# Performance work log

Measured on AMD Instinct MI355X. Metric: run time of the kernel, lower is better.

## Reference

```python
import jax, jax.numpy as jnp
import numpy as np

N = 100000   # nodes
E = 1600000  # edges
D = 128      # input feature dim
H = 128      # hidden dim
C = 40       # output classes


def _gcn_conv(x, W, b, src, dst, norm):
    # PyG GCNConv: h = x @ W; out_i = sum_j (d_i^-1/2 d_j^-1/2) h_j over in-edges,
    # including self-loops, then + bias. norm = deg^-1/2 with self-loop-augmented degree.
    h = x @ W                                    # [N, H]
    coef = norm[src] * norm[dst]                 # [E]
    agg = jax.ops.segment_sum(h[src] * coef[:, None], dst, num_segments=N)
    agg = agg + h * (norm * norm)[:, None]       # self-loop term
    return agg + b


def setup_inputs() -> dict:
    key = jax.random.key(0)
    ks = jax.random.split(key, 12)
    x = jax.random.normal(ks[0], (N, D), dtype=jnp.float32)
    edge_index = jax.random.randint(ks[1], (2, E), 0, N, dtype=jnp.int64)

    def lin(k, fan_in, fan_out):
        s = 1.0 / np.sqrt(fan_in)
        return jax.random.uniform(k, (fan_in, fan_out), jnp.float32, -s, s)

    return {
        "x": x,
        "edge_index": edge_index,
        "W1": lin(ks[2], D, H), "b1": jnp.zeros((H,), jnp.float32),
        "W2": lin(ks[3], H, H), "b2": jnp.zeros((H,), jnp.float32),
        "W3": lin(ks[4], H, H), "b3": jnp.zeros((H,), jnp.float32),
        "Wp1": lin(ks[5], H, H), "bp1": jnp.zeros((H,), jnp.float32),
        "Wp2": lin(ks[6], H, C), "bp2": jnp.zeros((C,), jnp.float32),
    }


def reference(x, edge_index, W1, b1, W2, b2, W3, b3, Wp1, bp1, Wp2, bp2):
    src, dst = edge_index[0], edge_index[1]
    # degree with self-loops (GCNConv adds self-loops by default)
    deg = jax.ops.segment_sum(jnp.ones((E,), jnp.float32), dst, num_segments=N) + 1.0
    norm = jax.lax.rsqrt(deg)                    # deg^-1/2

    h = x
    for W, b in ((W1, b1), (W2, b2), (W3, b3)):
        h = _gcn_conv(h, W, b, src, dst, norm)
        h = jax.nn.relu(h)
        # dropout is a no-op at inference / rate 0

    h = h @ Wp1 + bp1
    h = h @ Wp2 + bp2
    return jax.nn.log_softmax(h, axis=1)
```

## Files before the change

### kernel.cpp

```cpp
#include <hip/hip_runtime.h>
#include <hip/hip_bf16.h>
#include <math.h>


#define DH 128
#define NC 40
#define BN 256
#define MAXNB 512
#define CH 8192
#define ECAP 6144
#define SP 136

typedef __attribute__((ext_vector_type(8))) short bf16x8;
typedef __attribute__((ext_vector_type(4))) float f32x4;

__device__ __forceinline__ unsigned short f2bf(float f) {
    unsigned u = __float_as_uint(f);
    unsigned r = (u + 0x7fffu + ((u >> 16) & 1u)) >> 16;
    return (unsigned short)r;
}
__device__ __forceinline__ unsigned pack2(float lo, float hi) {
    return (unsigned)f2bf(lo) | ((unsigned)f2bf(hi) << 16);
}


__global__ __launch_bounds__(256) void bucket_hist(const int* __restrict__ dst, int E,
                                                   unsigned* __restrict__ bcnt) {
    __shared__ unsigned h[MAXNB];
    int tid = threadIdx.x;
    for (int i = tid; i < MAXNB; i += 256) h[i] = 0;
    __syncthreads();
    int e0 = blockIdx.x * CH;
    int e1 = min(e0 + CH, E);
    for (int i = e0 + tid; i < e1; i += 256)
        atomicAdd(&h[dst[i] >> 8], 1u);
    __syncthreads();
    for (int i = tid; i < MAXNB; i += 256)
        if (h[i]) atomicAdd(&bcnt[i], h[i]);
}

__global__ __launch_bounds__(256) void bucket_alloc(const unsigned* __restrict__ bcnt,
                                                    unsigned* __restrict__ bbase,
                                                    unsigned* __restrict__ bpos,
                                                    unsigned* __restrict__ cursor, int NB) {
    int i = blockIdx.x * 256 + threadIdx.x;
    if (i < NB) {
        unsigned c = bcnt[i];
        unsigned o = atomicAdd(cursor, c);
        bbase[i] = o;
        bpos[i] = o;
    }
}

__global__ __launch_bounds__(256) void bucket_scatter(const int* __restrict__ src,
                                                      const int* __restrict__ dst, int E,
                                                      unsigned* __restrict__ bpos,
                                                      unsigned* __restrict__ ebuf) {
    __shared__ unsigned hist[MAXNB];
    __shared__ unsigned lbase[MAXNB];
    __shared__ unsigned gbase[MAXNB];
    __shared__ unsigned cur[MAXNB];
    __shared__ unsigned sorted[CH];
    __shared__ unsigned short sbkt[CH];
    __shared__ unsigned total;

    int tid = threadIdx.x;
    int e0 = blockIdx.x * CH;
    int nE = min(CH, E - e0);

    for (int i = tid; i < MAXNB; i += 256) { hist[i] = 0; cur[i] = 0; }
    if (tid == 0) total = 0;
    __syncthreads();

    for (int i = tid; i < nE; i += 256)
        atomicAdd(&hist[dst[e0 + i] >> 8], 1u);
    __syncthreads();

    for (int i = tid; i < MAXNB; i += 256) {
        unsigned h = hist[i];
        lbase[i] = h ? atomicAdd(&total, h) : 0u;
        gbase[i] = h ? atomicAdd(&bpos[i], h) : 0u;
    }
    __syncthreads();

    for (int i = tid; i < nE; i += 256) {
        int s = src[e0 + i];
        int d = dst[e0 + i];
        unsigned b = (unsigned)d >> 8;
        unsigned r = atomicAdd(&cur[b], 1u);
        unsigned p = lbase[b] + r;
        sorted[p] = ((unsigned)s << 8) | ((unsigned)d & 255u);
        sbkt[p] = (unsigned short)b;
    }
    __syncthreads();

    for (int p = tid; p < nE; p += 256) {
        unsigned b = sbkt[p];
        ebuf[gbase[b] + (p - lbase[b])] = sorted[p];
    }
}


__global__ __launch_bounds__(256) void bucket_deg(const unsigned* __restrict__ ebuf,
                                                  const unsigned* __restrict__ bbase,
                                                  const unsigned* __restrict__ bcnt,
                                                  unsigned* __restrict__ cnt,
                                                  float* __restrict__ nrm,
                                                  unsigned* __restrict__ dh, int N) {
    __shared__ unsigned h[BN];
    __shared__ unsigned dhh[256];
    int b = blockIdx.x, tid = threadIdx.x;
    unsigned ebase = bbase[b], ecnt = bcnt[b];
    h[tid] = 0; dhh[tid] = 0;
    __syncthreads();
    for (unsigned i = tid; i < ecnt; i += 256)
        atomicAdd(&h[ebuf[ebase + i] & 255u], 1u);
    __syncthreads();
    int node = b * BN + tid;
    unsigned myh = h[tid];
    if (node < N) {
        cnt[node] = myh;
        nrm[node] = rsqrtf((float)myh + 1.0f);
        atomicAdd(&dhh[min(myh, 255u)], 1u);
    }
    __syncthreads();
    if (dhh[tid]) atomicAdd(&dh[tid], dhh[tid]);
}

__global__ __launch_bounds__(256) void deg_scan(const unsigned* __restrict__ dh,
                                                unsigned* __restrict__ binpos,
                                                unsigned* __restrict__ nstart0,
                                                unsigned* __restrict__ estart) {
    __shared__ unsigned s[256];
    int t = threadIdx.x;
    s[t] = dh[t];
    __syncthreads();
    unsigned ns = 0, es = 0;
    for (int d = t + 1; d < 256; ++d) { ns += s[d]; es += s[d] * (unsigned)d; }
    binpos[t] = ns;
    nstart0[t] = ns;
    estart[t] = es;
}

__global__ __launch_bounds__(256) void deg_scatter(const unsigned* __restrict__ cnt, int N,
                                                   unsigned* __restrict__ binpos,
                                                   const unsigned* __restrict__ nstart0,
                                                   const unsigned* __restrict__ estart,
                                                   int* __restrict__ perm,
                                                   unsigned* __restrict__ pd2,
                                                   unsigned* __restrict__ offN) {
    __shared__ unsigned h[256], base[256], cur[256], sns[256], ses[256];
    int t = threadIdx.x;
    h[t] = 0; cur[t] = 0; sns[t] = nstart0[t]; ses[t] = estart[t];
    __syncthreads();
    int i = blockIdx.x * 256 + t;
    unsigned d = 0;
    if (i < N) { d = min(cnt[i], 255u); atomicAdd(&h[d], 1u); }
    __syncthreads();
    if (h[t]) base[t] = atomicAdd(&binpos[t], h[t]);
    __syncthreads();
    if (i < N) {
        unsigned r = atomicAdd(&cur[d], 1u);
        unsigned idx = base[d] + r;
        unsigned off2 = ses[d] + (idx - sns[d]) * d;
        perm[idx] = i;
        pd2[idx] = (off2 << 9) | d;
        offN[i] = off2;
    }
}


__global__ __launch_bounds__(256) void bucket_fill(const unsigned* __restrict__ ebuf,
                                                   const unsigned* __restrict__ bbase,
                                                   const unsigned* __restrict__ bcnt,
                                                   const unsigned* __restrict__ offN,
                                                   int* __restrict__ csr, int N) {
    __shared__ unsigned h[BN], lb[BN], cur[BN], ofs[BN];
    __shared__ int lcsr[ECAP];
    __shared__ unsigned char snl[ECAP];
    __shared__ unsigned tot;

    int b = blockIdx.x, tid = threadIdx.x;
    unsigned ebase = bbase[b], ecnt = bcnt[b];
    int node = b * BN + tid;
    h[tid] = 0; cur[tid] = 0;
    ofs[tid] = (node < N) ? offN[node] : 0u;
    if (tid == 0) tot = 0;
    __syncthreads();

    for (unsigned i = tid; i < ecnt; i += 256)
        atomicAdd(&h[ebuf[ebase + i] & 255u], 1u);
    __syncthreads();

    unsigned myh = h[tid];
    lb[tid] = myh ? atomicAdd(&tot, myh) : 0u;
    __syncthreads();

    if (ecnt <= ECAP) {
        for (unsigned i = tid; i < ecnt; i += 256) {
            unsigned v = ebuf[ebase + i];
            unsigned nl = v & 255u;
            unsigned r = atomicAdd(&cur[nl], 1u);
            unsigned p = lb[nl] + r;
            lcsr[p] = (int)(v >> 8);
            snl[p] = (unsigned char)nl;
        }
        __syncthreads();
        for (unsigned i = tid; i < ecnt; i += 256) {
            unsigned nl = snl[i];
            csr[ofs[nl] + (i - lb[nl])] = lcsr[i];
        }
    } else {
        for (unsigned i = tid; i < ecnt; i += 256) {
            unsigned v = ebuf[ebase + i];
            unsigned nl = v & 255u;
            unsigned r = atomicAdd(&cur[nl], 1u);
            csr[ofs[nl] + r] = (int)(v >> 8);
        }
    }
}


__global__ __launch_bounds__(256) void prep_w(const float* __restrict__ W1,
                                              const float* __restrict__ W2,
                                              const float* __restrict__ W3,
                                              const float* __restrict__ Wp1,
                                              const float* __restrict__ bp1,
                                              const float* __restrict__ Wp2,
                                              const float* __restrict__ bp2,
                                              unsigned short* __restrict__ Wt,
                                              unsigned short* __restrict__ Wft,
                                              float* __restrict__ bfh) {
    int id = blockIdx.x * 256 + threadIdx.x;
    if (id < 3 * DH * DH) {
        int l = id >> 14, r = id & (DH * DH - 1);
        int k = r >> 7, n = r & 127;
        const float* W = (l == 0) ? W1 : (l == 1) ? W2 : W3;
        Wt[l * DH * DH + n * DH + k] = f2bf(W[k * DH + n]);
    } else if (id < 3 * DH * DH + 48 * DH) {
        int o = id - 3 * DH * DH;
        int c = o >> 7, k = o & 127;
        float acc = 0.f;
        if (c < NC)
            for (int j = 0; j < DH; ++j) acc += Wp1[k * DH + j] * Wp2[j * NC + c];
        Wft[c * DH + k] = f2bf(acc);
    } else if (id < 3 * DH * DH + 48 * DH + 48) {
        int c = id - 3 * DH * DH - 48 * DH;
        float acc = 0.f;
        if (c < NC) {
            acc = bp2[c];
            for (int j = 0; j < DH; ++j) acc += bp1[j] * Wp2[j * NC + c];
        }
        bfh[c] = acc;
    }
}


__global__ __launch_bounds__(256) void gemm_mfma_f32(const float* __restrict__ X,
                                                     const unsigned short* __restrict__ Wt,
                                                     const float* __restrict__ nrm,
                                                     unsigned short* __restrict__ outb,
                                                     int nrows) {
    const int tid = threadIdx.x;
    const int wave = tid >> 6;
    const int lane = tid & 63;
    const int m = lane & 15;
    const int quad = lane >> 4;
    const int rbase = blockIdx.x * 128 + wave * 32;

    union U8 { bf16x8 v; unsigned u[4]; };

    f32x4 acc[2][8];
#pragma unroll
    for (int rt = 0; rt < 2; ++rt)
#pragma unroll
        for (int ct = 0; ct < 8; ++ct) acc[rt][ct] = (f32x4){0.f, 0.f, 0.f, 0.f};

#pragma unroll
    for (int kt = 0; kt < 4; ++kt) {
        const int kof = kt * 32 + quad * 8;
        bf16x8 a[2], b[8];
#pragma unroll
        for (int rt = 0; rt < 2; ++rt) {
            int r = rbase + rt * 16 + m;
            r = (r < nrows) ? r : (nrows - 1);
            const float* p = X + (size_t)r * DH + kof;
            float4 u0 = *(const float4*)p;
            float4 u1 = *(const float4*)(p + 4);
            U8 t;
            t.u[0] = pack2(u0.x, u0.y);
            t.u[1] = pack2(u0.z, u0.w);
            t.u[2] = pack2(u1.x, u1.y);
            t.u[3] = pack2(u1.z, u1.w);
            a[rt] = t.v;
        }
#pragma unroll
        for (int ct = 0; ct < 8; ++ct)
            b[ct] = *(const bf16x8*)(Wt + (ct * 16 + m) * DH + kof);
#pragma unroll
        for (int rt = 0; rt < 2; ++rt)
#pragma unroll
            for (int ct = 0; ct < 8; ++ct)
                acc[rt][ct] = __builtin_amdgcn_mfma_f32_16x16x32_bf16(a[rt], b[ct], acc[rt][ct], 0, 0, 0);
    }

#pragma unroll
    for (int rt = 0; rt < 2; ++rt)
#pragma unroll
        for (int reg = 0; reg < 4; ++reg) {
            int r = rbase + rt * 16 + quad * 4 + reg;
            if (r < nrows) {
                float s = nrm[r];
#pragma unroll
                for (int ct = 0; ct < 8; ++ct)
                    outb[(size_t)r * DH + ct * 16 + m] = f2bf(acc[rt][ct][reg] * s);
            }
        }
}


__device__ __forceinline__ void bf8_add(float* acc, uint4 v) {
    acc[0] += __uint_as_float(v.x << 16);
    acc[1] += __uint_as_float(v.x & 0xffff0000u);
    acc[2] += __uint_as_float(v.y << 16);
    acc[3] += __uint_as_float(v.y & 0xffff0000u);
    acc[4] += __uint_as_float(v.z << 16);
    acc[5] += __uint_as_float(v.z & 0xffff0000u);
    acc[6] += __uint_as_float(v.w << 16);
    acc[7] += __uint_as_float(v.w & 0xffff0000u);
}

__device__ __forceinline__ void gather_phase(const uint4* __restrict__ Abf,
                                             const int* __restrict__ csr,
                                             const unsigned* __restrict__ pd2,
                                             const int* __restrict__ perm,
                                             const float* __restrict__ bias,
                                             unsigned short (*sA)[SP],
                                             int* snode, float* snrm, int N) {
    const int tid = threadIdx.x;
    const int g = tid >> 4;
    const int lane = tid & 15;
    const int idx = blockIdx.x * 16 + g;
    if (idx < N) {
        const unsigned pd = pd2[idx];
        const unsigned o = pd >> 9;
        const unsigned d = pd & 511u;
        const int node = perm[idx];

        float acc[8];
        {
            uint4 v = Abf[(size_t)node * 16 + lane];
            acc[0] = __uint_as_float(v.x << 16);
            acc[1] = __uint_as_float(v.x & 0xffff0000u);
            acc[2] = __uint_as_float(v.y << 16);
            acc[3] = __uint_as_float(v.y & 0xffff0000u);
            acc[4] = __uint_as_float(v.z << 16);
            acc[5] = __uint_as_float(v.z & 0xffff0000u);
            acc[6] = __uint_as_float(v.w << 16);
            acc[7] = __uint_as_float(v.w & 0xffff0000u);
        }

        unsigned e = 0;
        for (; e + 4 <= d; e += 4) {
            int s0 = csr[o + e + 0];
            int s1 = csr[o + e + 1];
            int s2 = csr[o + e + 2];
            int s3 = csr[o + e + 3];
            uint4 v0 = Abf[(size_t)s0 * 16 + lane];
            uint4 v1 = Abf[(size_t)s1 * 16 + lane];
            uint4 v2 = Abf[(size_t)s2 * 16 + lane];
            uint4 v3 = Abf[(size_t)s3 * 16 + lane];
            bf8_add(acc, v0);
            bf8_add(acc, v1);
            bf8_add(acc, v2);
            bf8_add(acc, v3);
        }
        for (; e < d; ++e) {
            int s = csr[o + e];
            uint4 v = Abf[(size_t)s * 16 + lane];
            bf8_add(acc, v);
        }

        float nm = rsqrtf((float)d + 1.0f);
        if (lane == 0) { snode[g] = node; snrm[g] = nm; }
        float4 b0 = *(const float4*)(bias + lane * 8);
        float4 b1 = *(const float4*)(bias + lane * 8 + 4);
        uint4 ov;
        ov.x = pack2(fmaxf(acc[0] * nm + b0.x, 0.f), fmaxf(acc[1] * nm + b0.y, 0.f));
        ov.y = pack2(fmaxf(acc[2] * nm + b0.z, 0.f), fmaxf(acc[3] * nm + b0.w, 0.f));
        ov.z = pack2(fmaxf(acc[4] * nm + b1.x, 0.f), fmaxf(acc[5] * nm + b1.y, 0.f));
        ov.w = pack2(fmaxf(acc[6] * nm + b1.z, 0.f), fmaxf(acc[7] * nm + b1.w, 0.f));
        *(uint4*)&sA[g][lane * 8] = ov;
    }
    __syncthreads();
}


__global__ __launch_bounds__(256) void agg_gemm(const uint4* __restrict__ Abf,
                                                const int* __restrict__ csr,
                                                const unsigned* __restrict__ pd2,
                                                const int* __restrict__ perm,
                                                const float* __restrict__ bias,
                                                const unsigned short* __restrict__ Wt,
                                                unsigned short* __restrict__ outb, int N) {
    __shared__ unsigned short sA[16][SP];
    __shared__ int snode[16];
    __shared__ float snrm[16];
    gather_phase(Abf, csr, pd2, perm, bias, sA, snode, snrm, N);

    const int tid = threadIdx.x;
    const int wave = tid >> 6;
    const int l64 = tid & 63;
    const int m = l64 & 15;
    const int quad = l64 >> 4;

    f32x4 acc[2];
    acc[0] = (f32x4){0.f, 0.f, 0.f, 0.f};
    acc[1] = (f32x4){0.f, 0.f, 0.f, 0.f};

#pragma unroll
    for (int kt = 0; kt < 4; ++kt) {
        const int kof = kt * 32 + quad * 8;
        bf16x8 a = *(const bf16x8*)&sA[m][kof];
#pragma unroll
        for (int c2 = 0; c2 < 2; ++c2) {
            const int ct = wave * 2 + c2;
            bf16x8 b = *(const bf16x8*)(Wt + (ct * 16 + m) * DH + kof);
            acc[c2] = __builtin_amdgcn_mfma_f32_16x16x32_bf16(a, b, acc[c2], 0, 0, 0);
        }
    }

#pragma unroll
    for (int reg = 0; reg < 4; ++reg) {
        int idx = blockIdx.x * 16 + quad * 4 + reg;
        if (idx < N) {
            int r = snode[quad * 4 + reg];
            float s = snrm[quad * 4 + reg];
#pragma unroll
            for (int c2 = 0; c2 < 2; ++c2)
                outb[(size_t)r * DH + (wave * 2 + c2) * 16 + m] = f2bf(acc[c2][reg] * s);
        }
    }
}


__global__ __launch_bounds__(256) void agg_head(const uint4* __restrict__ Abf,
                                                const int* __restrict__ csr,
                                                const unsigned* __restrict__ pd2,
                                                const int* __restrict__ perm,
                                                const float* __restrict__ bias,
                                                const unsigned short* __restrict__ Wft,
                                                const float* __restrict__ bfh,
                                                float* __restrict__ out, int N) {
    __shared__ unsigned short sA[16][SP];
    __shared__ int snode[16];
    __shared__ float snrm[16];
    gather_phase(Abf, csr, pd2, perm, bias, sA, snode, snrm, N);

    const int tid = threadIdx.x;
    if (tid >= 64) return;
    const int m = tid & 15;
    const int quad = tid >> 4;

    f32x4 acc[3];
#pragma unroll
    for (int ct = 0; ct < 3; ++ct) acc[ct] = (f32x4){0.f, 0.f, 0.f, 0.f};

#pragma unroll
    for (int kt = 0; kt < 4; ++kt) {
        const int kof = kt * 32 + quad * 8;
        bf16x8 a = *(const bf16x8*)&sA[m][kof];
#pragma unroll
        for (int ct = 0; ct < 3; ++ct) {
            bf16x8 b = *(const bf16x8*)(Wft + (ct * 16 + m) * DH + kof);
            acc[ct] = __builtin_amdgcn_mfma_f32_16x16x32_bf16(a, b, acc[ct], 0, 0, 0);
        }
    }

    float bias0 = bfh[m];
    float bias1 = bfh[16 + m];
    float bias2 = bfh[32 + m];

#pragma unroll
    for (int reg = 0; reg < 4; ++reg) {
        float v0 = acc[0][reg] + bias0;
        float v1 = acc[1][reg] + bias1;
        float v2 = (m < 8) ? (acc[2][reg] + bias2) : -1e30f;
        float mx = fmaxf(fmaxf(v0, v1), v2);
#pragma unroll
        for (int dlt = 1; dlt < 16; dlt <<= 1) mx = fmaxf(mx, __shfl_xor(mx, dlt));
        float s = __expf(v0 - mx) + __expf(v1 - mx) + ((m < 8) ? __expf(v2 - mx) : 0.f);
#pragma unroll
        for (int dlt = 1; dlt < 16; dlt <<= 1) s += __shfl_xor(s, dlt);
        float ls = mx + __logf(s);
        int idx = blockIdx.x * 16 + quad * 4 + reg;
        if (idx < N) {
            int r = snode[quad * 4 + reg];
            out[(size_t)r * NC + m] = v0 - ls;
            out[(size_t)r * NC + 16 + m] = v1 - ls;
            if (m < 8) out[(size_t)r * NC + 32 + m] = v2 - ls;
        }
    }
}


extern "C" void kernel_launch(void* const* d_in, const int* in_sizes, int n_in,
                              void* d_out, int out_size, void* d_ws, size_t ws_size,
                              hipStream_t stream) {
    const float* x   = (const float*)d_in[0];
    const int*   ei  = (const int*)d_in[1];
    const float* W1  = (const float*)d_in[2];
    const float* b1  = (const float*)d_in[3];
    const float* W2  = (const float*)d_in[4];
    const float* b2  = (const float*)d_in[5];
    const float* W3  = (const float*)d_in[6];
    const float* b3  = (const float*)d_in[7];
    const float* Wp1 = (const float*)d_in[8];
    const float* bp1 = (const float*)d_in[9];
    const float* Wp2 = (const float*)d_in[10];
    const float* bp2 = (const float*)d_in[11];
    float* out = (float*)d_out;

    const int N = in_sizes[0] / DH;
    const int E = in_sizes[1] / 2;
    const int* src = ei;
    const int* dst = ei + E;
    const int NB = (N + BN - 1) / BN;

    char* w = (char*)d_ws;
    unsigned short* Ab  = (unsigned short*)w; w += (size_t)N * DH * 2;
    unsigned short* Bb  = (unsigned short*)w; w += (size_t)N * DH * 2;
    int*      csr    = (int*)w;      w += (size_t)E * 4;
    unsigned* ebuf   = (unsigned*)w; w += (size_t)E * 4;
    unsigned* bcnt   = (unsigned*)w; w += MAXNB * 4;
    unsigned* cursor = (unsigned*)w; w += 16;
    unsigned* dh     = (unsigned*)w; w += 256 * 4;
    unsigned* bbase  = (unsigned*)w; w += MAXNB * 4;
    unsigned* bpos   = (unsigned*)w; w += MAXNB * 4;
    unsigned* binpos = (unsigned*)w; w += 256 * 4;
    unsigned* nstart0= (unsigned*)w; w += 256 * 4;
    unsigned* estart = (unsigned*)w; w += 256 * 4;
    unsigned* cnt    = (unsigned*)w; w += (size_t)N * 4;
    float*    nrm    = (float*)w;    w += (size_t)N * 4;
    unsigned* offN   = (unsigned*)w; w += (size_t)N * 4;
    unsigned* pd2    = (unsigned*)w; w += (size_t)((N + 31) & ~31) * 4;
    int*      perm   = (int*)w;      w += (size_t)((N + 31) & ~31) * 4;
    unsigned short* Wt  = (unsigned short*)w; w += 3 * DH * DH * 2;
    unsigned short* Wft = (unsigned short*)w; w += 48 * DH * 2;
    float*    bfh    = (float*)w;    w += 64 * 4;

    const int gC = (E + CH - 1) / CH;
    const int gN = (N + 255) / 256;

    hipMemsetAsync(bcnt, 0, MAXNB * 4 + 16 + 256 * 4, stream);
    bucket_hist   <<<gC, 256, 0, stream>>>(dst, E, bcnt);
    bucket_alloc  <<<(NB + 255) / 256, 256, 0, stream>>>(bcnt, bbase, bpos, cursor, NB);
    bucket_scatter<<<gC, 256, 0, stream>>>(src, dst, E, bpos, ebuf);
    bucket_deg    <<<NB, 256, 0, stream>>>(ebuf, bbase, bcnt, cnt, nrm, dh, N);
    deg_scan      <<<1, 256, 0, stream>>>(dh, binpos, nstart0, estart);
    deg_scatter   <<<gN, 256, 0, stream>>>(cnt, N, binpos, nstart0, estart, perm, pd2, offN);
    bucket_fill   <<<NB, 256, 0, stream>>>(ebuf, bbase, bcnt, offN, csr, N);
    prep_w<<<(3 * DH * DH + 48 * DH + 48 + 255) / 256, 256, 0, stream>>>(
        W1, W2, W3, Wp1, bp1, Wp2, bp2, Wt, Wft, bfh);

    const int gG = (N + 127) / 128;
    const int gF = (N + 15) / 16;

    gemm_mfma_f32<<<gG, 256, 0, stream>>>(x, Wt, nrm, Ab, N);
    agg_gemm<<<gF, 256, 0, stream>>>((const uint4*)Ab, csr, pd2, perm, b1,
                                     Wt + DH * DH, Bb, N);
    agg_gemm<<<gF, 256, 0, stream>>>((const uint4*)Bb, csr, pd2, perm, b2,
                                     Wt + 2 * DH * DH, Ab, N);
    agg_head<<<gF, 256, 0, stream>>>((const uint4*)Ab, csr, pd2, perm, b3,
                                     Wft, bfh, out, N);
}
```

Measured before the change: 418.0 us.

## Replace bucketed two-pass CSR build with direct global-atomic degree count and scatter

The old CSR build bucketed edges by destination block in shared memory, wrote an intermediate edge buffer, and then did per-bucket degree and fill passes. The new build counts degrees with global atomics per edge and scatters source indices into the CSR using an atomic cursor per node. This drops the ebuf round trip and several kernel launches. In exchange it relies on contended global atomics with random access, and neighbour order inside each row becomes nondeterministic, which can change float summation order. offN is now consumed as a cursor, so it ends pointing at row ends, while pd2 still holds the row starts.

```diff
diff --git a/kernel.cpp b/kernel.cpp
--- a/kernel.cpp
+++ b/kernel.cpp
@@ -5,10 +5,6 @@
 
 #define DH 128
 #define NC 40
-#define BN 256
-#define MAXNB 512
-#define CH 8192
-#define ECAP 6144
 #define SP 136
 
 typedef __attribute__((ext_vector_type(8))) short bf16x8;
@@ -24,107 +20,30 @@
 }
 
 
-__global__ __launch_bounds__(256) void bucket_hist(const int* __restrict__ dst, int E,
-                                                   unsigned* __restrict__ bcnt) {
-    __shared__ unsigned h[MAXNB];
-    int tid = threadIdx.x;
-    for (int i = tid; i < MAXNB; i += 256) h[i] = 0;
-    __syncthreads();
-    int e0 = blockIdx.x * CH;
-    int e1 = min(e0 + CH, E);
-    for (int i = e0 + tid; i < e1; i += 256)
-        atomicAdd(&h[dst[i] >> 8], 1u);
-    __syncthreads();
-    for (int i = tid; i < MAXNB; i += 256)
-        if (h[i]) atomicAdd(&bcnt[i], h[i]);
-}
-
-__global__ __launch_bounds__(256) void bucket_alloc(const unsigned* __restrict__ bcnt,
-                                                    unsigned* __restrict__ bbase,
-                                                    unsigned* __restrict__ bpos,
-                                                    unsigned* __restrict__ cursor, int NB) {
+__global__ __launch_bounds__(256) void edge_deg(const int* __restrict__ dst, int E,
+                                                unsigned* __restrict__ cnt) {
     int i = blockIdx.x * 256 + threadIdx.x;
-    if (i < NB) {
-        unsigned c = bcnt[i];
-        unsigned o = atomicAdd(cursor, c);
-        bbase[i] = o;
-        bpos[i] = o;
-    }
-}
-
-__global__ __launch_bounds__(256) void bucket_scatter(const int* __restrict__ src,
-                                                      const int* __restrict__ dst, int E,
-                                                      unsigned* __restrict__ bpos,
-                                                      unsigned* __restrict__ ebuf) {
-    __shared__ unsigned hist[MAXNB];
-    __shared__ unsigned lbase[MAXNB];
-    __shared__ unsigned gbase[MAXNB];
-    __shared__ unsigned cur[MAXNB];
-    __shared__ unsigned sorted[CH];
-    __shared__ unsigned short sbkt[CH];
-    __shared__ unsigned total;
-
-    int tid = threadIdx.x;
-    int e0 = blockIdx.x * CH;
-    int nE = min(CH, E - e0);
-
-    for (int i = tid; i < MAXNB; i += 256) { hist[i] = 0; cur[i] = 0; }
-    if (tid == 0) total = 0;
-    __syncthreads();
-
-    for (int i = tid; i < nE; i += 256)
-        atomicAdd(&hist[dst[e0 + i] >> 8], 1u);
-    __syncthreads();
-
-    for (int i = tid; i < MAXNB; i += 256) {
-        unsigned h = hist[i];
-        lbase[i] = h ? atomicAdd(&total, h) : 0u;
-        gbase[i] = h ? atomicAdd(&bpos[i], h) : 0u;
-    }
-    __syncthreads();
-
-    for (int i = tid; i < nE; i += 256) {
-        int s = src[e0 + i];
-        int d = dst[e0 + i];
-        unsigned b = (unsigned)d >> 8;
-        unsigned r = atomicAdd(&cur[b], 1u);
-        unsigned p = lbase[b] + r;
-        sorted[p] = ((unsigned)s << 8) | ((unsigned)d & 255u);
-        sbkt[p] = (unsigned short)b;
-    }
-    __syncthreads();
-
-    for (int p = tid; p < nE; p += 256) {
-        unsigned b = sbkt[p];
-        ebuf[gbase[b] + (p - lbase[b])] = sorted[p];
-    }
-}
-
-
-__global__ __launch_bounds__(256) void bucket_deg(const unsigned* __restrict__ ebuf,
-                                                  const unsigned* __restrict__ bbase,
-                                                  const unsigned* __restrict__ bcnt,
-                                                  unsigned* __restrict__ cnt,
+    int stride = gridDim.x * 256;
+    for (; i < E; i += stride)
+        atomicAdd(&cnt[dst[i]], 1u);
+}
+
+
+__global__ __launch_bounds__(256) void node_stats(const unsigned* __restrict__ cnt,
                                                   float* __restrict__ nrm,
                                                   unsigned* __restrict__ dh, int N) {
-    __shared__ unsigned h[BN];
     __shared__ unsigned dhh[256];
-    int b = blockIdx.x, tid = threadIdx.x;
-    unsigned ebase = bbase[b], ecnt = bcnt[b];
-    h[tid] = 0; dhh[tid] = 0;
-    __syncthreads();
-    for (unsigned i = tid; i < ecnt; i += 256)
-        atomicAdd(&h[ebuf[ebase + i] & 255u], 1u);
-    __syncthreads();
-    int node = b * BN + tid;
-    unsigned myh = h[tid];
-    if (node < N) {
-        cnt[node] = myh;
-        nrm[node] = rsqrtf((float)myh + 1.0f);
-        atomicAdd(&dhh[min(myh, 255u)], 1u);
-    }
-    __syncthreads();
-    if (dhh[tid]) atomicAdd(&dh[tid], dhh[tid]);
+    int t = threadIdx.x;
+    dhh[t] = 0;
+    __syncthreads();
+    int i = blockIdx.x * 256 + t;
+    if (i < N) {
+        unsigned c = cnt[i];
+        nrm[i] = rsqrtf((float)c + 1.0f);
+        atomicAdd(&dhh[min(c, 255u)], 1u);
+    }
+    __syncthreads();
+    if (dhh[t]) atomicAdd(&dh[t], dhh[t]);
 }
 
 __global__ __launch_bounds__(256) void deg_scan(const unsigned* __restrict__ dh,
@@ -170,53 +89,15 @@
 }
 
 
-__global__ __launch_bounds__(256) void bucket_fill(const unsigned* __restrict__ ebuf,
-                                                   const unsigned* __restrict__ bbase,
-                                                   const unsigned* __restrict__ bcnt,
-                                                   const unsigned* __restrict__ offN,
-                                                   int* __restrict__ csr, int N) {
-    __shared__ unsigned h[BN], lb[BN], cur[BN], ofs[BN];
-    __shared__ int lcsr[ECAP];
-    __shared__ unsigned char snl[ECAP];
-    __shared__ unsigned tot;
-
-    int b = blockIdx.x, tid = threadIdx.x;
-    unsigned ebase = bbase[b], ecnt = bcnt[b];
-    int node = b * BN + tid;
-    h[tid] = 0; cur[tid] = 0;
-    ofs[tid] = (node < N) ? offN[node] : 0u;
-    if (tid == 0) tot = 0;
-    __syncthreads();
-
-    for (unsigned i = tid; i < ecnt; i += 256)
-        atomicAdd(&h[ebuf[ebase + i] & 255u], 1u);
-    __syncthreads();
-
-    unsigned myh = h[tid];
-    lb[tid] = myh ? atomicAdd(&tot, myh) : 0u;
-    __syncthreads();
-
-    if (ecnt <= ECAP) {
-        for (unsigned i = tid; i < ecnt; i += 256) {
-            unsigned v = ebuf[ebase + i];
-            unsigned nl = v & 255u;
-            unsigned r = atomicAdd(&cur[nl], 1u);
-            unsigned p = lb[nl] + r;
-            lcsr[p] = (int)(v >> 8);
-            snl[p] = (unsigned char)nl;
-        }
-        __syncthreads();
-        for (unsigned i = tid; i < ecnt; i += 256) {
-            unsigned nl = snl[i];
-            csr[ofs[nl] + (i - lb[nl])] = lcsr[i];
-        }
-    } else {
-        for (unsigned i = tid; i < ecnt; i += 256) {
-            unsigned v = ebuf[ebase + i];
-            unsigned nl = v & 255u;
-            unsigned r = atomicAdd(&cur[nl], 1u);
-            csr[ofs[nl] + r] = (int)(v >> 8);
-        }
+__global__ __launch_bounds__(256) void csr_scatter(const int* __restrict__ src,
+                                                   const int* __restrict__ dst, int E,
+                                                   unsigned* __restrict__ offN,
+                                                   int* __restrict__ csr) {
+    int i = blockIdx.x * 256 + threadIdx.x;
+    int stride = gridDim.x * 256;
+    for (; i < E; i += stride) {
+        unsigned p = atomicAdd(&offN[dst[i]], 1u);
+        csr[p] = src[i];
     }
 }
 
@@ -525,23 +406,17 @@
     const int E = in_sizes[1] / 2;
     const int* src = ei;
     const int* dst = ei + E;
-    const int NB = (N + BN - 1) / BN;
 
     char* w = (char*)d_ws;
     unsigned short* Ab  = (unsigned short*)w; w += (size_t)N * DH * 2;
     unsigned short* Bb  = (unsigned short*)w; w += (size_t)N * DH * 2;
     int*      csr    = (int*)w;      w += (size_t)E * 4;
-    unsigned* ebuf   = (unsigned*)w; w += (size_t)E * 4;
-    unsigned* bcnt   = (unsigned*)w; w += MAXNB * 4;
-    unsigned* cursor = (unsigned*)w; w += 16;
+    unsigned* cnt    = (unsigned*)w; w += (size_t)N * 4;
     unsigned* dh     = (unsigned*)w; w += 256 * 4;
-    unsigned* bbase  = (unsigned*)w; w += MAXNB * 4;
-    unsigned* bpos   = (unsigned*)w; w += MAXNB * 4;
+    float*    nrm    = (float*)w;    w += (size_t)N * 4;
     unsigned* binpos = (unsigned*)w; w += 256 * 4;
     unsigned* nstart0= (unsigned*)w; w += 256 * 4;
     unsigned* estart = (unsigned*)w; w += 256 * 4;
-    unsigned* cnt    = (unsigned*)w; w += (size_t)N * 4;
-    float*    nrm    = (float*)w;    w += (size_t)N * 4;
     unsigned* offN   = (unsigned*)w; w += (size_t)N * 4;
     unsigned* pd2    = (unsigned*)w; w += (size_t)((N + 31) & ~31) * 4;
     int*      perm   = (int*)w;      w += (size_t)((N + 31) & ~31) * 4;
@@ -549,17 +424,16 @@
     unsigned short* Wft = (unsigned short*)w; w += 48 * DH * 2;
     float*    bfh    = (float*)w;    w += 64 * 4;
 
-    const int gC = (E + CH - 1) / CH;
     const int gN = (N + 255) / 256;
-
-    hipMemsetAsync(bcnt, 0, MAXNB * 4 + 16 + 256 * 4, stream);
-    bucket_hist   <<<gC, 256, 0, stream>>>(dst, E, bcnt);
-    bucket_alloc  <<<(NB + 255) / 256, 256, 0, stream>>>(bcnt, bbase, bpos, cursor, NB);
-    bucket_scatter<<<gC, 256, 0, stream>>>(src, dst, E, bpos, ebuf);
-    bucket_deg    <<<NB, 256, 0, stream>>>(ebuf, bbase, bcnt, cnt, nrm, dh, N);
-    deg_scan      <<<1, 256, 0, stream>>>(dh, binpos, nstart0, estart);
-    deg_scatter   <<<gN, 256, 0, stream>>>(cnt, N, binpos, nstart0, estart, perm, pd2, offN);
-    bucket_fill   <<<NB, 256, 0, stream>>>(ebuf, bbase, bcnt, offN, csr, N);
+    const int gE = min((E + 255) / 256, 2048);
+
+    hipMemsetAsync(cnt, 0, (size_t)N * 4 + 256 * 4, stream);
+
+    edge_deg   <<<gE, 256, 0, stream>>>(dst, E, cnt);
+    node_stats <<<gN, 256, 0, stream>>>(cnt, nrm, dh, N);
+    deg_scan   <<<1, 256, 0, stream>>>(dh, binpos, nstart0, estart);
+    deg_scatter<<<gN, 256, 0, stream>>>(cnt, N, binpos, nstart0, estart, perm, pd2, offN);
+    csr_scatter<<<gE, 256, 0, stream>>>(src, dst, E, offN, csr);
     prep_w<<<(3 * DH * DH + 48 * DH + 48 + 255) / 256, 256, 0, stream>>>(
         W1, W2, W3, Wp1, bp1, Wp2, bp2, Wt, Wft, bfh);
 
```

Result: slower. 551.3 us (+31.9%).
